# Performance work log

Measured on AMD Instinct MI355X. Metric: run time of the kernel, lower is better.

The kernel has to match this reference:

```python
import jax, jax.numpy as jnp
import numpy as np

B, C, H, W = 2, 128, 64, 64
EPS = 1e-5


def setup_inputs() -> dict:
    key = jax.random.key(0)
    ks = jax.random.split(key, 8)
    sc = 1.0 / np.sqrt(C)
    inp = {
        "x": jax.random.normal(ks[0], (B, C, H, W, 2), jnp.float32),
        # naive complex BN affine params: per-channel, per-component (real/imag)
        "bn_w": jnp.ones((C, 2), jnp.float32),
        "bn_b": jnp.zeros((C, 2), jnp.float32),
        # complex 1x1 conv weights: (out_c, in_c, 2) -> [..,0]=W_real, [..,1]=W_imag
        "wq": jax.random.normal(ks[1], (C, C, 2), jnp.float32) * sc,
        "bq": jnp.zeros((C, 2), jnp.float32),
        "wk": jax.random.normal(ks[2], (C, C, 2), jnp.float32) * sc,
        "bk": jnp.zeros((C, 2), jnp.float32),
        "wv": jax.random.normal(ks[3], (C, C, 2), jnp.float32) * sc,
        "bv": jnp.zeros((C, 2), jnp.float32),
        "gamma": jnp.float32(0.05),
    }
    return inp


def _complex_bn(x, w, b):
    # naive complex BN: normalize real and imag independently per channel
    # x: (B,C,H,W,2); stats over (B,H,W) per (C, component)
    mean = x.mean(axis=(0, 2, 3), keepdims=True)
    var = x.var(axis=(0, 2, 3), keepdims=True)
    xn = (x - mean) * jax.lax.rsqrt(var + EPS)
    return xn * w[None, :, None, None, :] + b[None, :, None, None, :]


def _complex_conv1x1(x, w, b):
    # x: (B,C,H,W,2); w: (O,C,2); b: (O,2)
    xr, xi = x[..., 0], x[..., 1]
    wr, wi = w[..., 0], w[..., 1]
    yr = jnp.einsum('oc,bchw->bohw', wr, xr) - jnp.einsum('oc,bchw->bohw', wi, xi)
    yi = jnp.einsum('oc,bchw->bohw', wr, xi) + jnp.einsum('oc,bchw->bohw', wi, xr)
    yr = yr + b[:, 0][None, :, None, None]
    yi = yi + b[:, 1][None, :, None, None]
    return jnp.stack([yr, yi], axis=-1)


def _attention(x, wq, bq, wk, bk, wv, bv, gamma):
    scale = C ** (-0.5)
    N = H * W
    # q,k,v: (B,C,H,W,2) -> (B,C,N,2) -> (B,N,C,2)
    to_tokens = lambda t: t.reshape(B, C, N, 2).transpose(0, 2, 1, 3)
    q = to_tokens(_complex_conv1x1(x, wq, bq))
    k = to_tokens(_complex_conv1x1(x, wk, bk))
    v = to_tokens(_complex_conv1x1(x, wv, bv))

    qr, qi = q[..., 0], q[..., 1]          # (B,N,C)
    kr, ki = k[..., 0], -k[..., 1]         # conjugate of k
    # k_t = conj(k) with token/channel axes swapped -> (B,C,N)
    ktr = kr.transpose(0, 2, 1)
    kti = ki.transpose(0, 2, 1)

    # complex matmul q @ k_t -> only the real part is used downstream
    attn_real = jnp.einsum('bnc,bcm->bnm', qr, ktr) - jnp.einsum('bnc,bcm->bnm', qi, kti)
    attn_w = jax.nn.softmax(attn_real * scale, axis=-1)  # (B,N,N)
    # dropout = identity (eval mode)

    # attn is purely real -> complex matmul reduces to two real matmuls
    out_r = jnp.einsum('bnm,bmc->bnc', attn_w, v[..., 0])
    out_i = jnp.einsum('bnm,bmc->bnc', attn_w, v[..., 1])
    out = jnp.stack([out_r, out_i], axis=-1)              # (B,N,C,2)
    out = out.transpose(0, 2, 1, 3).reshape(B, C, H, W, 2)
    return x + gamma * out


def reference(x, bn_w, bn_b, wq, bq, wk, bk, wv, bv, gamma):
    xn = _complex_bn(x, bn_w, bn_b)
    return _attention(xn, wq, bq, wk, bk, wv, bv, gamma)
```

## Files before the change

kernel.cpp:

```cpp
#include <hip/hip_runtime.h>
#include <hip/hip_bf16.h>

typedef __bf16 bf16_t;
typedef __bf16 bf16x8 __attribute__((ext_vector_type(8)));
typedef float  f32x4  __attribute__((ext_vector_type(4)));

#define MFMA16(A,B,C) __builtin_amdgcn_mfma_f32_16x16x32_bf16((A),(B),(C),0,0,0)

constexpr int Bn = 2, Cc = 128, Hh = 64, Wd = 64;
constexpr int N  = Hh * Wd;
constexpr int T  = Bn * N;
constexpr int D  = 2 * Cc;
constexpr int NSP = 4;
constexpr float EPS = 1e-5f;
constexpr float SCL = 0.08838834764831845f * 1.4426950408889634f;

__device__ __forceinline__ int tfrag(int row, int ch) {
    return (((ch >> 5) * 4 + (row >> 4)) << 10) +
           ((((ch >> 3) & 3) * 16 + (row & 15)) << 4) + (ch & 7) * 2;
}
__device__ __forceinline__ int vfrag(int ch, int key) {
    return (((key >> 5) * 16 + (ch >> 4)) << 10) +
           ((((key >> 3) & 3) * 16 + (ch & 15)) << 4) + (key & 7) * 2;
}

__device__ __forceinline__ void gl16(const void* g, void* l) {
    __builtin_amdgcn_global_load_lds(
        (const __attribute__((address_space(1))) void*)g,
        (__attribute__((address_space(3))) void*)l, 16, 0, 0);
}

__global__ void k_pre(const float* __restrict__ x, float4* __restrict__ part,
                      const float* __restrict__ wq, const float* __restrict__ wk,
                      const float* __restrict__ wv, const float* __restrict__ bq,
                      const float* __restrict__ bk, const float* __restrict__ bv,
                      char* __restrict__ Wg, float* __restrict__ bt) {
    int tid = threadIdx.x;
    if (blockIdx.x < 512) {
        int bid = blockIdx.x;
        int q = bid >> 7, c = bid & 127;
        float sr = 0.f, si = 0.f, qr = 0.f, qi = 0.f;
        for (int b = 0; b < Bn; ++b) {
            const float2* p = (const float2*)x + (size_t)(b * Cc + c) * N + q * 1024;
            for (int i = tid; i < 1024; i += 256) {
                float2 v = p[i];
                sr += v.x; si += v.y; qr += v.x * v.x; qi += v.y * v.y;
            }
        }
        #pragma unroll
        for (int d = 32; d >= 1; d >>= 1) {
            sr += __shfl_xor(sr, d); si += __shfl_xor(si, d);
            qr += __shfl_xor(qr, d); qi += __shfl_xor(qi, d);
        }
        __shared__ float red[4][4];
        int w = tid >> 6;
        if ((tid & 63) == 0) { red[w][0] = sr; red[w][1] = si; red[w][2] = qr; red[w][3] = qi; }
        __syncthreads();
        if (tid == 0) {
            part[c * 4 + q] = make_float4(red[0][0] + red[1][0] + red[2][0] + red[3][0],
                                          red[0][1] + red[1][1] + red[2][1] + red[3][1],
                                          red[0][2] + red[1][2] + red[2][2] + red[3][2],
                                          red[0][3] + red[1][3] + red[2][3] + red[3][3]);
        }
    } else {
        int o = blockIdx.x - 512;
        int k = tid;
        int proj = o >> 8, oc = o & 255;
        const float* wsrc = proj == 0 ? wq : (proj == 1 ? wk : wv);
        const float* bsrc = proj == 0 ? bq : (proj == 1 ? bk : bv);
        int co = oc >> 7, oo = oc & 127;
        int c = k & 127, kc = k >> 7;
        float val;
        if (co == 0) val = (kc == 0) ? wsrc[(oo * 128 + c) * 2 + 0] : -wsrc[(oo * 128 + c) * 2 + 1];
        else         val = (kc == 0) ? wsrc[(oo * 128 + c) * 2 + 1] :  wsrc[(oo * 128 + c) * 2 + 0];
        int tile = o >> 6, row = o & 63;
        *(bf16_t*)(Wg + (size_t)tile * 32768 + tfrag(row, k)) = (bf16_t)val;
        if (k == 0) bt[o] = bsrc[oo * 2 + co];
    }
}

__global__ void k_norm(const float* __restrict__ x, const float4* __restrict__ part,
                       const float* __restrict__ bn_w, const float* __restrict__ bn_b,
                       char* __restrict__ XNg) {
    __shared__ float4 ssl[128];
    __shared__ __align__(16) char Tsh[32768];
    int blk = blockIdx.x;
    int b = blk >> 6, hw0 = (blk & 63) * 64;
    int tid = threadIdx.x;
    if (tid < 128) {
        float4 p0 = part[tid * 4 + 0], p1 = part[tid * 4 + 1];
        float4 p2 = part[tid * 4 + 2], p3 = part[tid * 4 + 3];
        float sr = p0.x + p1.x + p2.x + p3.x, si = p0.y + p1.y + p2.y + p3.y;
        float qr = p0.z + p1.z + p2.z + p3.z, qi = p0.w + p1.w + p2.w + p3.w;
        const float inv = 1.0f / (float)(Bn * N);
        float mr = sr * inv, mi = si * inv;
        float vr = qr * inv - mr * mr, vi = qi * inv - mi * mi;
        float scr = bn_w[tid * 2 + 0] * rsqrtf(vr + EPS);
        float sci = bn_w[tid * 2 + 1] * rsqrtf(vi + EPS);
        ssl[tid] = make_float4(scr, bn_b[tid * 2 + 0] - mr * scr,
                               sci, bn_b[tid * 2 + 1] - mi * sci);
    }
    __syncthreads();
    const float2* xin = (const float2*)x;
    #pragma unroll
    for (int it = 0; it < 32; ++it) {
        int idx = it * 256 + tid;
        int c = idx >> 6, hw = idx & 63;
        size_t gi = (size_t)(b * Cc + c) * N + hw0 + hw;
        float2 v = xin[gi];
        float4 s = ssl[c];
        *(bf16_t*)(Tsh + tfrag(hw, c))       = (bf16_t)(v.x * s.x + s.y);
        *(bf16_t*)(Tsh + tfrag(hw, c + 128)) = (bf16_t)(v.y * s.z + s.w);
    }
    __syncthreads();
    #pragma unroll
    for (int it = 0; it < 8; ++it) {
        int idx = it * 256 + tid;
        *(uint4*)(XNg + (size_t)blk * 32768 + idx * 16) = *(const uint4*)(Tsh + idx * 16);
    }
}

__global__ __launch_bounds__(256) void k_qkv(const char* __restrict__ XNg,
        const char* __restrict__ Wg, const float* __restrict__ bt,
        char* __restrict__ Qg, char* __restrict__ Kg, char* __restrict__ Vg) {
    __shared__ __align__(16) char Xsh[32768];
    __shared__ __align__(16) char Wsh[32768];
    int mx = blockIdx.x, ny = blockIdx.y;
    int tid = threadIdx.x;
    int w = tid >> 6, lane = tid & 63, n15 = lane & 15, quad = lane >> 4;
    const char* xs = XNg + (size_t)mx * 32768;
    const char* wsp = Wg + (size_t)ny * 32768;
    #pragma unroll
    for (int i = 0; i < 8; ++i) {
        int off = (w * 8 + i) * 1024 + lane * 16;
        gl16(xs + off, Xsh + off);
        gl16(wsp + off, Wsh + off);
    }
    __syncthreads();
    f32x4 acc[4] = {};
    #pragma unroll
    for (int ks = 0; ks < 8; ++ks) {
        bf16x8 a = *(const bf16x8*)(Xsh + (ks * 4 + w) * 1024 + lane * 16);
        #pragma unroll
        for (int t = 0; t < 4; ++t) {
            bf16x8 bw = *(const bf16x8*)(Wsh + (ks * 4 + t) * 1024 + lane * 16);
            acc[t] = MFMA16(a, bw, acc[t]);
        }
    }
    int proj = ny >> 2;
    int jb = (ny & 3) * 64;
    #pragma unroll
    for (int t = 0; t < 4; ++t) {
        int j = jb + t * 16 + n15;
        float bias = bt[ny * 64 + t * 16 + n15];
        #pragma unroll
        for (int r = 0; r < 4; ++r) {
            int tk = mx * 64 + w * 16 + quad * 4 + r;
            float v = acc[t][r] + bias;
            int bb = tk >> 12, n = tk & (N - 1);
            if (proj == 0) {
                *(bf16_t*)(Qg + (size_t)(tk >> 6) * 32768 + tfrag(tk & 63, j)) = (bf16_t)v;
            } else {
                size_t tb = (size_t)(bb * 64 + (n >> 6)) * 32768;
                if (proj == 1) *(bf16_t*)(Kg + tb + tfrag(n & 63, j)) = (bf16_t)v;
                else           *(bf16_t*)(Vg + tb + vfrag(j, n & 63)) = (bf16_t)v;
            }
        }
    }
}

__global__ __launch_bounds__(256, 2) void k_attn(const char* __restrict__ Qg,
        const char* __restrict__ Kg, const char* __restrict__ Vg,
        bf16_t* __restrict__ Opb, float* __restrict__ Lp) {
    __shared__ __align__(16) char Ksh[32768];
    __shared__ __align__(16) char Vsh[32768 + 1024];
    __shared__ __align__(16) char Psh[8192];
    int bid = blockIdx.x;
    int qt = bid & 63, sp = (bid >> 6) & 3, b = bid >> 8;
    int tid = threadIdx.x;
    int w = tid >> 6, lane = tid & 63, n15 = lane & 15, quad = lane >> 4;
    int r = w >> 1, h = w & 1;

    if (tid < 64) {
        uint4 ones; ones.x = ones.y = ones.z = ones.w = 0x3F803F80u;
        *(uint4*)(Vsh + 32768 + tid * 16) = ones;
    }

    bf16x8 qf[2][8];
    const char* qb = Qg + (size_t)(b * 64 + qt) * 32768;
    #pragma unroll
    for (int g = 0; g < 2; ++g)
        #pragma unroll
        for (int ks = 0; ks < 8; ++ks)
            qf[g][ks] = *(const bf16x8*)(qb + (ks * 4 + r * 2 + g) * 1024 + lane * 16);

    f32x4 o[2][8] = {};
    f32x4 l_[2] = {};

    for (int kt = 0; kt < 16; ++kt) {
        size_t tb = (size_t)(b * 64 + sp * 16 + kt) * 32768;
        __syncthreads();
        #pragma unroll
        for (int i = 0; i < 8; ++i) {
            int off = (w * 8 + i) * 1024 + lane * 16;
            gl16(Kg + tb + off, Ksh + off);
            gl16(Vg + tb + off, Vsh + off);
        }
        __syncthreads();

        f32x4 s[2][2] = {};
        #pragma unroll
        for (int ks = 0; ks < 8; ++ks) {
            #pragma unroll
            for (int c = 0; c < 2; ++c) {
                bf16x8 kf = *(const bf16x8*)(Ksh + (ks * 4 + h * 2 + c) * 1024 + lane * 16);
                s[0][c] = MFMA16(qf[0][ks], kf, s[0][c]);
                s[1][c] = MFMA16(qf[1][ks], kf, s[1][c]);
            }
        }
        #pragma unroll
        for (int g = 0; g < 2; ++g)
            #pragma unroll
            for (int c = 0; c < 2; ++c)
                #pragma unroll
                for (int ri = 0; ri < 4; ++ri) {
                    float p = __builtin_amdgcn_exp2f(s[g][c][ri] * SCL);
                    *(bf16_t*)(Psh + (h * 4 + r * 2 + g) * 1024 +
                               ((c * 2 + (n15 >> 3)) * 16 + quad * 4 + ri) * 16 +
                               (n15 & 7) * 2) = (bf16_t)p;
                }
        __syncthreads();
        #pragma unroll
        for (int k2 = 0; k2 < 2; ++k2) {
            bf16x8 pa0 = *(const bf16x8*)(Psh + (k2 * 4 + r * 2 + 0) * 1024 + lane * 16);
            bf16x8 pa1 = *(const bf16x8*)(Psh + (k2 * 4 + r * 2 + 1) * 1024 + lane * 16);
            bf16x8 onef = *(const bf16x8*)(Vsh + 32768 + lane * 16);
            l_[0] = MFMA16(pa0, onef, l_[0]);
            l_[1] = MFMA16(pa1, onef, l_[1]);
            #pragma unroll
            for (int ct = 0; ct < 8; ++ct) {
                bf16x8 vf = *(const bf16x8*)(Vsh + (k2 * 16 + h * 8 + ct) * 1024 + lane * 16);
                o[0][ct] = MFMA16(pa0, vf, o[0][ct]);
                o[1][ct] = MFMA16(pa1, vf, o[1][ct]);
            }
        }
    }
    int tok0 = b * N + qt * 64 + r * 32;
    #pragma unroll
    for (int g = 0; g < 2; ++g) {
        #pragma unroll
        for (int ct = 0; ct < 8; ++ct)
            #pragma unroll
            for (int ri = 0; ri < 4; ++ri)
                Opb[((size_t)sp * T + tok0 + g * 16 + quad * 4 + ri) * D +
                    h * 128 + ct * 16 + n15] = (bf16_t)o[g][ct][ri];
        if (h == 0 && n15 == 0) {
            #pragma unroll
            for (int ri = 0; ri < 4; ++ri)
                Lp[sp * T + tok0 + g * 16 + quad * 4 + ri] = l_[g][ri];
        }
    }
}

__global__ void k_comb(const bf16_t* __restrict__ Opb, const float* __restrict__ Lp,
                       const float4* __restrict__ part, const float* __restrict__ bn_w,
                       const float* __restrict__ bn_b, const float* __restrict__ x,
                       const float* __restrict__ gamma, float* __restrict__ out) {
    __shared__ float4 ssl[128];
    __shared__ float wts[32];
    __shared__ float Ot[256 * 33];
    int blk = blockIdx.x;
    int b = blk >> 7, hw0 = (blk & 127) * 32;
    int tok0 = b * N + hw0;
    int tid = threadIdx.x;
    if (tid < 128) {
        float4 p0 = part[tid * 4 + 0], p1 = part[tid * 4 + 1];
        float4 p2 = part[tid * 4 + 2], p3 = part[tid * 4 + 3];
        float sr = p0.x + p1.x + p2.x + p3.x, si = p0.y + p1.y + p2.y + p3.y;
        float qr = p0.z + p1.z + p2.z + p3.z, qi = p0.w + p1.w + p2.w + p3.w;
        const float inv = 1.0f / (float)(Bn * N);
        float mr = sr * inv, mi = si * inv;
        float vr = qr * inv - mr * mr, vi = qi * inv - mi * mi;
        float scr = bn_w[tid * 2 + 0] * rsqrtf(vr + EPS);
        float sci = bn_w[tid * 2 + 1] * rsqrtf(vi + EPS);
        ssl[tid] = make_float4(scr, bn_b[tid * 2 + 0] - mr * scr,
                               sci, bn_b[tid * 2 + 1] - mi * sci);
    }
    if (tid < 32) {
        float Z = 0.f;
        #pragma unroll
        for (int s = 0; s < NSP; ++s) Z += Lp[s * T + tok0 + tid];
        wts[tid] = gamma[0] / Z;
    }
    __syncthreads();
    #pragma unroll
    for (int i = 0; i < 4; ++i) {
        int idx = i * 256 + tid;
        int tk = idx >> 5, chunk = idx & 31;
        size_t base = (size_t)(tok0 + tk) * D + chunk * 8;
        float acc[8] = {};
        #pragma unroll
        for (int s = 0; s < NSP; ++s) {
            bf16x8 v = *(const bf16x8*)(Opb + (size_t)s * T * D + base);
            #pragma unroll
            for (int j = 0; j < 8; ++j) acc[j] += (float)v[j];
        }
        float ww = wts[tk];
        #pragma unroll
        for (int j = 0; j < 8; ++j) Ot[(chunk * 8 + j) * 33 + tk] = acc[j] * ww;
    }
    __syncthreads();
    const float2* xin = (const float2*)x;
    float2* xo = (float2*)out;
    #pragma unroll
    for (int i = 0; i < 16; ++i) {
        int linear = i * 256 + tid;
        int c = linear >> 5, hwo = linear & 31;
        size_t idx = (size_t)(b * Cc + c) * N + hw0 + hwo;
        float2 v = xin[idx];
        float4 s = ssl[c];
        float2 res;
        res.x = v.x * s.x + s.y + Ot[c * 33 + hwo];
        res.y = v.y * s.z + s.w + Ot[(128 + c) * 33 + hwo];
        xo[idx] = res;
    }
}

extern "C" void kernel_launch(void* const* d_in, const int* in_sizes, int n_in,
                              void* d_out, int out_size, void* d_ws, size_t ws_size,
                              hipStream_t stream) {
    const float* x    = (const float*)d_in[0];
    const float* bn_w = (const float*)d_in[1];
    const float* bn_b = (const float*)d_in[2];
    const float* wq   = (const float*)d_in[3];
    const float* bq   = (const float*)d_in[4];
    const float* wk   = (const float*)d_in[5];
    const float* bk   = (const float*)d_in[6];
    const float* wv   = (const float*)d_in[7];
    const float* bv   = (const float*)d_in[8];
    const float* gam  = (const float*)d_in[9];
    float* out = (float*)d_out;

    char* ws = (char*)d_ws;
    size_t off = 0;
    auto alloc = [&](size_t bytes) -> void* {
        void* p = ws + off;
        off += (bytes + 255) & ~(size_t)255;
        return p;
    };
    float4* part = (float4*)alloc(512 * sizeof(float4));
    char*   XNg  = (char*)alloc((size_t)128 * 32768);
    char*   Wg   = (char*)alloc((size_t)12 * 32768);
    float*  bt   = (float*)alloc(768 * 4);
    char*   Qg   = (char*)alloc((size_t)128 * 32768);
    char*   Kg   = (char*)alloc((size_t)128 * 32768);
    char*   Vg   = (char*)alloc((size_t)128 * 32768);
    bf16_t* Opb  = (bf16_t*)alloc((size_t)NSP * T * D * 2);
    float*  Lp   = (float*)alloc((size_t)NSP * T * 4);

    k_pre<<<1280, 256, 0, stream>>>(x, part, wq, wk, wv, bq, bk, bv, Wg, bt);
    k_norm<<<128, 256, 0, stream>>>(x, part, bn_w, bn_b, XNg);
    k_qkv<<<dim3(128, 12), 256, 0, stream>>>(XNg, Wg, bt, Qg, Kg, Vg);
    k_attn<<<512, 256, 0, stream>>>(Qg, Kg, Vg, Opb, Lp);
    k_comb<<<256, 256, 0, stream>>>(Opb, Lp, part, bn_w, bn_b, x, gam, out);
}
```

Measured before the change: 151.7 us.

## Fuse BN into QKV, fold softmax scale into Wq, double-buffer attention K/V tiles

The BN-normalize kernel is removed; each QKV block now normalizes its x tile directly into LDS, which drops the XN workspace round trip and one launch but repeats the normalization 12 times per token tile. The softmax scale is folded into the Q weights and bias, so the exp no longer needs a multiply. The attention loop now walks 32-key tiles with double-buffered K/V in LDS, prefetching the next tile while the current one is computed. The all-ones fragment is kept in registers instead of LDS. Smaller tiles mean more loop iterations and barriers, but each one moves less data and the loads overlap compute.

```diff
diff --git a/kernel.cpp b/kernel.cpp
--- a/kernel.cpp
+++ b/kernel.cpp
@@ -2,6 +2,7 @@
 #include <hip/hip_bf16.h>
 
 typedef __bf16 bf16_t;
+typedef __bf16 bf16x2 __attribute__((ext_vector_type(2)));
 typedef __bf16 bf16x8 __attribute__((ext_vector_type(8)));
 typedef float  f32x4  __attribute__((ext_vector_type(4)));
 
@@ -19,8 +20,12 @@
     return (((ch >> 5) * 4 + (row >> 4)) << 10) +
            ((((ch >> 3) & 3) * 16 + (row & 15)) << 4) + (ch & 7) * 2;
 }
-__device__ __forceinline__ int vfrag(int ch, int key) {
-    return (((key >> 5) * 16 + (ch >> 4)) << 10) +
+__device__ __forceinline__ int kfrag32(int key, int ch) {
+    return (((ch >> 5) * 2 + (key >> 4)) << 10) +
+           ((((ch >> 3) & 3) * 16 + (key & 15)) << 4) + (ch & 7) * 2;
+}
+__device__ __forceinline__ int vfrag32(int ch, int key) {
+    return ((ch >> 4) << 10) +
            ((((key >> 3) & 3) * 16 + (ch & 15)) << 4) + (key & 7) * 2;
 }
 
@@ -73,20 +78,30 @@
         float val;
         if (co == 0) val = (kc == 0) ? wsrc[(oo * 128 + c) * 2 + 0] : -wsrc[(oo * 128 + c) * 2 + 1];
         else         val = (kc == 0) ? wsrc[(oo * 128 + c) * 2 + 1] :  wsrc[(oo * 128 + c) * 2 + 0];
+        float fs = (proj == 0) ? SCL : 1.0f;
         int tile = o >> 6, row = o & 63;
-        *(bf16_t*)(Wg + (size_t)tile * 32768 + tfrag(row, k)) = (bf16_t)val;
-        if (k == 0) bt[o] = bsrc[oo * 2 + co];
-    }
-}
-
-__global__ void k_norm(const float* __restrict__ x, const float4* __restrict__ part,
-                       const float* __restrict__ bn_w, const float* __restrict__ bn_b,
-                       char* __restrict__ XNg) {
+        *(bf16_t*)(Wg + (size_t)tile * 32768 + tfrag(row, k)) = (bf16_t)(val * fs);
+        if (k == 0) bt[o] = bsrc[oo * 2 + co] * fs;
+    }
+}
+
+__global__ __launch_bounds__(256) void k_qkv(const float* __restrict__ x,
+        const float4* __restrict__ part, const float* __restrict__ bn_w,
+        const float* __restrict__ bn_b, const char* __restrict__ Wg,
+        const float* __restrict__ bt,
+        char* __restrict__ Qg, char* __restrict__ Kg, char* __restrict__ Vg) {
+    __shared__ __align__(16) char Xsh[32768];
+    __shared__ __align__(16) char Wsh[32768];
     __shared__ float4 ssl[128];
-    __shared__ __align__(16) char Tsh[32768];
-    int blk = blockIdx.x;
-    int b = blk >> 6, hw0 = (blk & 63) * 64;
+    int mx = blockIdx.x, ny = blockIdx.y;
     int tid = threadIdx.x;
+    int w = tid >> 6, lane = tid & 63, n15 = lane & 15, quad = lane >> 4;
+    const char* wsp = Wg + (size_t)ny * 32768;
+    #pragma unroll
+    for (int i = 0; i < 8; ++i) {
+        int off = (w * 8 + i) * 1024 + lane * 16;
+        gl16(wsp + off, Wsh + off);
+    }
     if (tid < 128) {
         float4 p0 = part[tid * 4 + 0], p1 = part[tid * 4 + 1];
         float4 p2 = part[tid * 4 + 2], p3 = part[tid * 4 + 3];
@@ -101,40 +116,20 @@
                                sci, bn_b[tid * 2 + 1] - mi * sci);
     }
     __syncthreads();
+    int b = mx >> 6, hw0 = (mx & 63) * 64;
     const float2* xin = (const float2*)x;
     #pragma unroll
-    for (int it = 0; it < 32; ++it) {
+    for (int it = 0; it < 16; ++it) {
         int idx = it * 256 + tid;
-        int c = idx >> 6, hw = idx & 63;
-        size_t gi = (size_t)(b * Cc + c) * N + hw0 + hw;
-        float2 v = xin[gi];
-        float4 s = ssl[c];
-        *(bf16_t*)(Tsh + tfrag(hw, c))       = (bf16_t)(v.x * s.x + s.y);
-        *(bf16_t*)(Tsh + tfrag(hw, c + 128)) = (bf16_t)(v.y * s.z + s.w);
-    }
-    __syncthreads();
-    #pragma unroll
-    for (int it = 0; it < 8; ++it) {
-        int idx = it * 256 + tid;
-        *(uint4*)(XNg + (size_t)blk * 32768 + idx * 16) = *(const uint4*)(Tsh + idx * 16);
-    }
-}
-
-__global__ __launch_bounds__(256) void k_qkv(const char* __restrict__ XNg,
-        const char* __restrict__ Wg, const float* __restrict__ bt,
-        char* __restrict__ Qg, char* __restrict__ Kg, char* __restrict__ Vg) {
-    __shared__ __align__(16) char Xsh[32768];
-    __shared__ __align__(16) char Wsh[32768];
-    int mx = blockIdx.x, ny = blockIdx.y;
-    int tid = threadIdx.x;
-    int w = tid >> 6, lane = tid & 63, n15 = lane & 15, quad = lane >> 4;
-    const char* xs = XNg + (size_t)mx * 32768;
-    const char* wsp = Wg + (size_t)ny * 32768;
-    #pragma unroll
-    for (int i = 0; i < 8; ++i) {
-        int off = (w * 8 + i) * 1024 + lane * 16;
-        gl16(xs + off, Xsh + off);
-        gl16(wsp + off, Wsh + off);
+        int cp = idx >> 6, hw = idx & 63;
+        size_t gi = (size_t)(b * Cc + cp * 2) * N + hw0 + hw;
+        float2 v0 = xin[gi], v1 = xin[gi + N];
+        float4 s0 = ssl[cp * 2], s1 = ssl[cp * 2 + 1];
+        bf16x2 pr, pi;
+        pr[0] = (bf16_t)(v0.x * s0.x + s0.y); pr[1] = (bf16_t)(v1.x * s1.x + s1.y);
+        pi[0] = (bf16_t)(v0.y * s0.z + s0.w); pi[1] = (bf16_t)(v1.y * s1.z + s1.w);
+        *(bf16x2*)(Xsh + tfrag(hw, cp * 2))       = pr;
+        *(bf16x2*)(Xsh + tfrag(hw, cp * 2 + 128)) = pi;
     }
     __syncthreads();
     f32x4 acc[4] = {};
@@ -161,9 +156,9 @@
             if (proj == 0) {
                 *(bf16_t*)(Qg + (size_t)(tk >> 6) * 32768 + tfrag(tk & 63, j)) = (bf16_t)v;
             } else {
-                size_t tb = (size_t)(bb * 64 + (n >> 6)) * 32768;
-                if (proj == 1) *(bf16_t*)(Kg + tb + tfrag(n & 63, j)) = (bf16_t)v;
-                else           *(bf16_t*)(Vg + tb + vfrag(j, n & 63)) = (bf16_t)v;
+                size_t tb = (size_t)(bb * 128 + (n >> 5)) * 16384;
+                if (proj == 1) *(bf16_t*)(Kg + tb + kfrag32(n & 31, j)) = (bf16_t)v;
+                else           *(bf16_t*)(Vg + tb + vfrag32(j, n & 31)) = (bf16_t)v;
             }
         }
     }
@@ -172,20 +167,15 @@
 __global__ __launch_bounds__(256, 2) void k_attn(const char* __restrict__ Qg,
         const char* __restrict__ Kg, const char* __restrict__ Vg,
         bf16_t* __restrict__ Opb, float* __restrict__ Lp) {
-    __shared__ __align__(16) char Ksh[32768];
-    __shared__ __align__(16) char Vsh[32768 + 1024];
-    __shared__ __align__(16) char Psh[8192];
+    __shared__ __align__(16) char Ksh[2][16384];
+    __shared__ __align__(16) char Vsh[2][16384];
+    __shared__ __align__(16) char Psh[2][4096];
     int bid = blockIdx.x;
     int qt = bid & 63, sp = (bid >> 6) & 3, b = bid >> 8;
     int tid = threadIdx.x;
     int w = tid >> 6, lane = tid & 63, n15 = lane & 15, quad = lane >> 4;
     int r = w >> 1, h = w & 1;
 
-    if (tid < 64) {
-        uint4 ones; ones.x = ones.y = ones.z = ones.w = 0x3F803F80u;
-        *(uint4*)(Vsh + 32768 + tid * 16) = ones;
-    }
-
     bf16x8 qf[2][8];
     const char* qb = Qg + (size_t)(b * 64 + qt) * 32768;
     #pragma unroll
@@ -194,55 +184,63 @@
         for (int ks = 0; ks < 8; ++ks)
             qf[g][ks] = *(const bf16x8*)(qb + (ks * 4 + r * 2 + g) * 1024 + lane * 16);
 
+    bf16x8 onev;
+    #pragma unroll
+    for (int j = 0; j < 8; ++j) onev[j] = (bf16_t)1.0f;
+
     f32x4 o[2][8] = {};
-    f32x4 l_[2] = {};
-
-    for (int kt = 0; kt < 16; ++kt) {
-        size_t tb = (size_t)(b * 64 + sp * 16 + kt) * 32768;
+    f32x4 l2[2] = {};
+
+    int tbase = b * 128 + sp * 32;
+    {
+        const char* kb = Kg + (size_t)tbase * 16384;
+        const char* vb = Vg + (size_t)tbase * 16384;
+        #pragma unroll
+        for (int i = 0; i < 4; ++i) {
+            int off = (w * 4 + i) * 1024 + lane * 16;
+            gl16(kb + off, Ksh[0] + off);
+            gl16(vb + off, Vsh[0] + off);
+        }
+    }
+    for (int kt = 0; kt < 32; ++kt) {
+        int p = kt & 1;
         __syncthreads();
-        #pragma unroll
-        for (int i = 0; i < 8; ++i) {
-            int off = (w * 8 + i) * 1024 + lane * 16;
-            gl16(Kg + tb + off, Ksh + off);
-            gl16(Vg + tb + off, Vsh + off);
-        }
+        f32x4 s[2] = {};
+        #pragma unroll
+        for (int ks = 0; ks < 8; ++ks) {
+            bf16x8 kf = *(const bf16x8*)(Ksh[p] + (ks * 2 + h) * 1024 + lane * 16);
+            s[0] = MFMA16(qf[0][ks], kf, s[0]);
+            s[1] = MFMA16(qf[1][ks], kf, s[1]);
+        }
+        #pragma unroll
+        for (int g = 0; g < 2; ++g)
+            #pragma unroll
+            for (int ri = 0; ri < 4; ++ri) {
+                float pv = __builtin_amdgcn_exp2f(s[g][ri]);
+                *(bf16_t*)(Psh[p] + (r * 2 + g) * 1024 +
+                           (h * 2 + (n15 >> 3)) * 256 + (quad * 4 + ri) * 16 +
+                           (n15 & 7) * 2) = (bf16_t)pv;
+            }
         __syncthreads();
-
-        f32x4 s[2][2] = {};
-        #pragma unroll
-        for (int ks = 0; ks < 8; ++ks) {
-            #pragma unroll
-            for (int c = 0; c < 2; ++c) {
-                bf16x8 kf = *(const bf16x8*)(Ksh + (ks * 4 + h * 2 + c) * 1024 + lane * 16);
-                s[0][c] = MFMA16(qf[0][ks], kf, s[0][c]);
-                s[1][c] = MFMA16(qf[1][ks], kf, s[1][c]);
+        if (kt < 31) {
+            const char* kb = Kg + (size_t)(tbase + kt + 1) * 16384;
+            const char* vb = Vg + (size_t)(tbase + kt + 1) * 16384;
+            #pragma unroll
+            for (int i = 0; i < 4; ++i) {
+                int off = (w * 4 + i) * 1024 + lane * 16;
+                gl16(kb + off, Ksh[p ^ 1] + off);
+                gl16(vb + off, Vsh[p ^ 1] + off);
             }
         }
-        #pragma unroll
-        for (int g = 0; g < 2; ++g)
-            #pragma unroll
-            for (int c = 0; c < 2; ++c)
-                #pragma unroll
-                for (int ri = 0; ri < 4; ++ri) {
-                    float p = __builtin_amdgcn_exp2f(s[g][c][ri] * SCL);
-                    *(bf16_t*)(Psh + (h * 4 + r * 2 + g) * 1024 +
-                               ((c * 2 + (n15 >> 3)) * 16 + quad * 4 + ri) * 16 +
-                               (n15 & 7) * 2) = (bf16_t)p;
-                }
-        __syncthreads();
-        #pragma unroll
-        for (int k2 = 0; k2 < 2; ++k2) {
-            bf16x8 pa0 = *(const bf16x8*)(Psh + (k2 * 4 + r * 2 + 0) * 1024 + lane * 16);
-            bf16x8 pa1 = *(const bf16x8*)(Psh + (k2 * 4 + r * 2 + 1) * 1024 + lane * 16);
-            bf16x8 onef = *(const bf16x8*)(Vsh + 32768 + lane * 16);
-            l_[0] = MFMA16(pa0, onef, l_[0]);
-            l_[1] = MFMA16(pa1, onef, l_[1]);
-            #pragma unroll
-            for (int ct = 0; ct < 8; ++ct) {
-                bf16x8 vf = *(const bf16x8*)(Vsh + (k2 * 16 + h * 8 + ct) * 1024 + lane * 16);
-                o[0][ct] = MFMA16(pa0, vf, o[0][ct]);
-                o[1][ct] = MFMA16(pa1, vf, o[1][ct]);
-            }
+        bf16x8 pa0 = *(const bf16x8*)(Psh[p] + (r * 2 + 0) * 1024 + lane * 16);
+        bf16x8 pa1 = *(const bf16x8*)(Psh[p] + (r * 2 + 1) * 1024 + lane * 16);
+        l2[0] = MFMA16(pa0, onev, l2[0]);
+        l2[1] = MFMA16(pa1, onev, l2[1]);
+        #pragma unroll
+        for (int ct = 0; ct < 8; ++ct) {
+            bf16x8 vf = *(const bf16x8*)(Vsh[p] + (h * 8 + ct) * 1024 + lane * 16);
+            o[0][ct] = MFMA16(pa0, vf, o[0][ct]);
+            o[1][ct] = MFMA16(pa1, vf, o[1][ct]);
         }
     }
     int tok0 = b * N + qt * 64 + r * 32;
@@ -257,7 +255,7 @@
         if (h == 0 && n15 == 0) {
             #pragma unroll
             for (int ri = 0; ri < 4; ++ri)
-                Lp[sp * T + tok0 + g * 16 + quad * 4 + ri] = l_[g][ri];
+                Lp[sp * T + tok0 + g * 16 + quad * 4 + ri] = l2[g][ri];
         }
     }
 }
@@ -349,18 +347,16 @@
         return p;
     };
     float4* part = (float4*)alloc(512 * sizeof(float4));
-    char*   XNg  = (char*)alloc((size_t)128 * 32768);
     char*   Wg   = (char*)alloc((size_t)12 * 32768);
     float*  bt   = (float*)alloc(768 * 4);
     char*   Qg   = (char*)alloc((size_t)128 * 32768);
-    char*   Kg   = (char*)alloc((size_t)128 * 32768);
-    char*   Vg   = (char*)alloc((size_t)128 * 32768);
+    char*   Kg   = (char*)alloc((size_t)256 * 16384);
+    char*   Vg   = (char*)alloc((size_t)256 * 16384);
     bf16_t* Opb  = (bf16_t*)alloc((size_t)NSP * T * D * 2);
     float*  Lp   = (float*)alloc((size_t)NSP * T * 4);
 
     k_pre<<<1280, 256, 0, stream>>>(x, part, wq, wk, wv, bq, bk, bv, Wg, bt);
-    k_norm<<<128, 256, 0, stream>>>(x, part, bn_w, bn_b, XNg);
-    k_qkv<<<dim3(128, 12), 256, 0, stream>>>(XNg, Wg, bt, Qg, Kg, Vg);
+    k_qkv<<<dim3(128, 12), 256, 0, stream>>>(x, part, bn_w, bn_b, Wg, bt, Qg, Kg, Vg);
     k_attn<<<512, 256, 0, stream>>>(Qg, Kg, Vg, Opb, Lp);
     k_comb<<<256, 256, 0, stream>>>(Opb, Lp, part, bn_w, bn_b, x, gam, out);
 }
```

New measurement: 153.9 us. Within noise of the previous version (+1.4%).
